# Kernel optimization log

Measured on AMD Instinct MI355X. Metric: run time of the kernel, lower is better.

## Reference

```python
import jax, jax.numpy as jnp
import numpy as np

N = 500_000      # total points
B = 64           # graphs in batch
D_IN = 64        # input feature dim (conv.in_tensor_reps.dim)
D_HID = 128      # EdgeConv MLP hidden
D_OUT = 128      # EdgeConv MLP out


def setup_inputs() -> dict:
    key = jax.random.key(0)
    k = jax.random.split(key, 8)
    x = jax.random.normal(k[0], (N, D_IN), jnp.float32)
    pos = jax.random.normal(k[1], (N, 3), jnp.float32)
    batch = jnp.sort(jax.random.randint(k[2], (N,), 0, B, dtype=jnp.int32))
    lframes = jax.random.normal(k[3], (N, 3, 3), jnp.float32)
    fan1 = 2 * D_IN + 3
    W1 = jax.random.normal(k[4], (fan1, D_HID), jnp.float32) / np.sqrt(fan1)
    b1 = jnp.zeros((D_HID,), jnp.float32)
    W2 = jax.random.normal(k[5], (D_HID, D_OUT), jnp.float32) / np.sqrt(D_HID)
    b2 = jnp.zeros((D_OUT,), jnp.float32)
    return {"x": x, "pos": pos, "batch": batch, "lframes": lframes,
            "W1": W1, "b1": b1, "W2": W2, "b2": b2}


def reference(x, pos, batch, lframes, W1, b1, W2, b2):
    n = pos.shape[0]
    # scatter-mean: center of mass per graph
    counts = jax.ops.segment_sum(jnp.ones((n,), pos.dtype), batch, num_segments=B)
    coms = jax.ops.segment_sum(pos, batch, num_segments=B) / jnp.maximum(counts, 1.0)[:, None]
    # distance of each point to its graph's COM
    dist = jnp.linalg.norm(pos - coms[batch], axis=-1)
    # scatter-min argmin per graph (first occurrence, like torch_scatter.scatter_min)
    min_d = jax.ops.segment_min(dist, batch, num_segments=B)
    node_ids = jnp.arange(n, dtype=jnp.int32)
    cand = jnp.where(dist <= min_d[batch], node_ids, n)
    idx = jnp.minimum(jax.ops.segment_min(cand, batch, num_segments=B), n - 1)  # [B]
    # gathers for the destination (center) nodes
    x_dst = x[idx]          # [B, D_IN]
    pos_dst = pos[idx]      # [B, 3]
    lframes_dst = lframes[idx]  # [B, 3, 3]
    # EdgeConv over edge_index = [arange(N) -> batch]:
    # message_e = MLP([x_dst_i, x_src_j - x_dst_i, pos_j - pos_i]), max-aggregated per graph
    xd = x_dst[batch]                      # [N, D_IN]
    feat = jnp.concatenate([xd, x - xd, pos - pos_dst[batch]], axis=-1)  # [N, 2*D_IN+3]
    h = jax.nn.relu(feat @ W1 + b1)        # [N, D_HID]
    msg = h @ W2 + b2                      # [N, D_OUT]
    out = jax.ops.segment_max(msg, batch, num_segments=B)  # [B, D_OUT]
    return out, pos_dst, batch[idx], lframes_dst
```

## Files before the change

kernel.cpp:

```cpp
#include <hip/hip_runtime.h>
#include <hip/hip_bf16.h>

#define NPTS 500000
#define NGR  64
#define TR   128
#define NT2  ((NPTS + TR - 1) / TR)
#define GRID2 1024

typedef __bf16 bf16x8 __attribute__((ext_vector_type(8)));
typedef float f32x4 __attribute__((ext_vector_type(4)));
typedef unsigned int u32x4 __attribute__((ext_vector_type(4)));

#define OFF_OUTACC 6144
#define OFF_CBIAS  38912
#define OFF_W1PT   71680
#define OFF_W1AT   73728
#define OFF_W2T    90112

__device__ __forceinline__ unsigned mapf(float f) {
    union { float f; unsigned u; } v; v.f = f;
    return ((int)v.u >= 0) ? (v.u | 0x80000000u) : ~v.u;
}

#define GLOAD_LDS16(g, l) __builtin_amdgcn_global_load_lds(                 \
    (__attribute__((address_space(1))) void*)(g),                           \
    (__attribute__((address_space(3))) void*)(l), 16, 0, 0)

__global__ __launch_bounds__(1024) void k_pre(
                      const float* __restrict__ pos,
                      const int* __restrict__ batch,
                      const float* __restrict__ x,
                      const float* __restrict__ W1,
                      const float* __restrict__ b1,
                      const float* __restrict__ W2,
                      const float* __restrict__ lfr,
                      unsigned short* __restrict__ W1aT,
                      unsigned short* __restrict__ W2T,
                      float* __restrict__ W1pT,
                      unsigned* __restrict__ outacc,
                      float* __restrict__ cbias,
                      float* __restrict__ outf) {
    __shared__ double sd[16][3];
    __shared__ unsigned long long sk[16];
    __shared__ double scom[3];
    __shared__ int sid;
    __shared__ float sposd[3];
    __shared__ float sp[4][128];
    __shared__ int sse[2];

    int g = blockIdx.x, t = threadIdx.x;
    int lane = t & 63, wv = t >> 6;

    {
        int i = g * 1024 + t;
        if (i < 8192) {
            outacc[i] = 0u;
            int n = i >> 6, k = i & 63;
            unsigned short v = (unsigned short)(__builtin_bit_cast(unsigned, (float)(__bf16)W1[(64 + k) * 128 + n]) >> 16);
            W1aT[i ^ ((n & 7) << 3)] = v;
        } else if (i < 8192 + 16384) {
            int j = i - 8192; int n = j >> 7, k = j & 127;
            unsigned short v = (unsigned short)(__builtin_bit_cast(unsigned, (float)(__bf16)W2[k * 128 + n]) >> 16);
            W2T[j ^ ((n & 7) << 3)] = v;
        } else if (i < 8192 + 16384 + 512) {
            int j = i - 24576; int n = j >> 2, q = j & 3;
            W1pT[j] = (q < 3) ? W1[(128 + q) * 128 + n] : 0.f;
        }
    }

    if (t < 2) {
        int target = g + t;
        int lo = 0, hi = NPTS;
        while (lo < hi) {
            int mid = (lo + hi) >> 1;
            if (batch[mid] < target) lo = mid + 1; else hi = mid;
        }
        sse[t] = lo;
    }
    __syncthreads();
    int s = sse[0], e = sse[1];

    double sx = 0.0, sy = 0.0, sz = 0.0;
    for (int i = s + t; i < e; i += 1024) {
        sx += (double)pos[i * 3 + 0];
        sy += (double)pos[i * 3 + 1];
        sz += (double)pos[i * 3 + 2];
    }
    #pragma unroll
    for (int m = 1; m < 64; m <<= 1) {
        sx += __shfl_xor(sx, m);
        sy += __shfl_xor(sy, m);
        sz += __shfl_xor(sz, m);
    }
    if (lane == 0) { sd[wv][0] = sx; sd[wv][1] = sy; sd[wv][2] = sz; }
    __syncthreads();
    if (t == 0) {
        double ax = 0.0, ay = 0.0, az = 0.0;
        for (int q = 0; q < 16; ++q) { ax += sd[q][0]; ay += sd[q][1]; az += sd[q][2]; }
        double cnt = (double)(e - s);
        double rc = 1.0 / (cnt > 1.0 ? cnt : 1.0);
        scom[0] = ax * rc; scom[1] = ay * rc; scom[2] = az * rc;
    }
    __syncthreads();
    double cx = scom[0], cy = scom[1], cz = scom[2];

    unsigned long long key = ~0ULL;
    for (int i = s + t; i < e; i += 1024) {
        double dx = (double)pos[i * 3 + 0] - cx;
        double dy = (double)pos[i * 3 + 1] - cy;
        double dz = (double)pos[i * 3 + 2] - cz;
        double d2 = __builtin_fma(dx, dx, __builtin_fma(dy, dy, dz * dz));
        unsigned long long b = __builtin_bit_cast(unsigned long long, d2);
        unsigned long long k2 = (b & ~0xFFFFFULL) | (unsigned long long)i;
        key = k2 < key ? k2 : key;
    }
    #pragma unroll
    for (int m = 1; m < 64; m <<= 1) {
        unsigned long long o = __shfl_xor(key, m);
        key = o < key ? o : key;
    }
    if (lane == 0) sk[wv] = key;
    __syncthreads();
    if (t == 0) {
        unsigned long long k = sk[0];
        for (int q = 1; q < 16; ++q) if (sk[q] < k) k = sk[q];
        int id = (int)(k & 0xFFFFFULL);
        if (id > NPTS - 1) id = NPTS - 1;
        sid = id;
    }
    __syncthreads();
    int id = sid;

    if (t < 3) {
        float p = pos[id * 3 + t];
        sposd[t] = p;
        outf[8192 + g * 3 + t] = p;
    }
    if (t == 4) outf[8192 + 192 + g] = (float)batch[id];
    if (t < 9) outf[8192 + 256 + g * 9 + t] = lfr[id * 9 + t];

    if (t < 512) {
        int c = t & 127, p = t >> 7;
        float part = 0.f;
        #pragma unroll
        for (int kq = 0; kq < 16; ++kq) {
            int k = p * 16 + kq;
            float xd = x[id * 64 + k];
            part += xd * (W1[k * 128 + c] - W1[(64 + k) * 128 + c]);
        }
        sp[p][c] = part;
    }
    __syncthreads();
    if (t < 128) {
        int c = t;
        float sv = b1[c] + sp[0][c] + sp[1][c] + sp[2][c] + sp[3][c];
        sv -= sposd[0] * W1[128 * 128 + c] + sposd[1] * W1[129 * 128 + c] + sposd[2] * W1[130 * 128 + c];
        cbias[g * 128 + c] = sv;
    }
}

__global__ __launch_bounds__(512, 2) void k_main(
    const float* __restrict__ x,
    const float* __restrict__ pos,
    const int* __restrict__ batch,
    const unsigned short* __restrict__ W1aT,
    const unsigned short* __restrict__ W2T,
    const float* __restrict__ W1pT,
    const float* __restrict__ cbias,
    unsigned* __restrict__ outacc)
{
    __shared__ alignas(16) unsigned char smem[81920];

    const int tid  = threadIdx.x;
    const int w    = tid >> 6;
    const int lane = tid & 63;
    const int quad = lane >> 4;
    const int mr   = lane & 15;

    #pragma unroll
    for (int i = 0; i < 6; ++i)
        GLOAD_LDS16((const char*)W1aT + (i * 512 + tid) * 16,
                    (char*)smem + (i * 512 + tid) * 16);

    bf16x8 bfrE[8];
    #pragma unroll
    for (int t8 = 0; t8 < 8; ++t8) {
        f32x4 wp = *(const f32x4*)(W1pT + (t8 * 16 + mr) * 4);
        bf16x8 e = (bf16x8){0, 0, 0, 0, 0, 0, 0, 0};
        if (quad == 0) { e[0] = (__bf16)wp[0]; e[1] = (__bf16)wp[1]; e[2] = (__bf16)wp[2]; }
        bfrE[t8] = e;
    }

    __syncthreads();

    const unsigned short* sW1 = (const unsigned short*)smem;
    const unsigned short* sW2 = (const unsigned short*)(smem + 16384);
    __bf16* hsb = (__bf16*)(smem + 49152) + w * 2048;
    const unsigned short* hss = (const unsigned short*)hsb;

    for (int t = blockIdx.x; t < NT2; t += GRID2) {
        const int row0 = t * TR + 16 * w;

        f32x4 av0, av1, av2, av3;
        {
            int gr2 = row0 + mr; if (gr2 > NPTS - 1) gr2 = NPTS - 1;
            const float* xp = x + (size_t)gr2 * 64 + quad * 8;
            av0 = *(const f32x4*)(xp);
            av1 = *(const f32x4*)(xp + 4);
            av2 = *(const f32x4*)(xp + 32);
            av3 = *(const f32x4*)(xp + 36);
        }

        int rowg[4]; bool rowv[4];
        #pragma unroll
        for (int r = 0; r < 4; ++r) {
            int gr = row0 + quad * 4 + r;
            rowv[r] = (gr < NPTS);
            rowg[r] = batch[gr < NPTS ? gr : NPTS - 1];
        }
        int gf = batch[row0 < NPTS ? row0 : NPTS - 1];
        int rl = row0 + 15; if (rl > NPTS - 1) rl = NPTS - 1;
        int gl = batch[rl];
        float cb0[8];
        #pragma unroll
        for (int t8 = 0; t8 < 8; ++t8) cb0[t8] = cbias[gf * 128 + t8 * 16 + mr];
        bf16x8 aE = (bf16x8){0, 0, 0, 0, 0, 0, 0, 0};
        {
            int gp = row0 + mr; if (gp > NPTS - 1) gp = NPTS - 1;
            if (quad == 0) {
                aE[0] = (__bf16)pos[gp * 3 + 0];
                aE[1] = (__bf16)pos[gp * 3 + 1];
                aE[2] = (__bf16)pos[gp * 3 + 2];
            }
        }

        bf16x8 afr0, afr1;
        afr0[0] = (__bf16)av0[0]; afr0[1] = (__bf16)av0[1]; afr0[2] = (__bf16)av0[2]; afr0[3] = (__bf16)av0[3];
        afr0[4] = (__bf16)av1[0]; afr0[5] = (__bf16)av1[1]; afr0[6] = (__bf16)av1[2]; afr0[7] = (__bf16)av1[3];
        afr1[0] = (__bf16)av2[0]; afr1[1] = (__bf16)av2[1]; afr1[2] = (__bf16)av2[2]; afr1[3] = (__bf16)av2[3];
        afr1[4] = (__bf16)av3[0]; afr1[5] = (__bf16)av3[1]; afr1[6] = (__bf16)av3[2]; afr1[7] = (__bf16)av3[3];

        f32x4 acc[8];
        #pragma unroll
        for (int t8 = 0; t8 < 8; ++t8) acc[t8] = (f32x4){0.f, 0.f, 0.f, 0.f};
        #pragma unroll
        for (int t8 = 0; t8 < 8; ++t8) {
            int n = t8 * 16 + mr;
            int sw = (n & 7) << 3;
            bf16x8 bv0 = __builtin_bit_cast(bf16x8, *(const u32x4*)(sW1 + ((n * 64 + quad * 8) ^ sw)));
            bf16x8 bv1 = __builtin_bit_cast(bf16x8, *(const u32x4*)(sW1 + ((n * 64 + 32 + quad * 8) ^ sw)));
            acc[t8] = __builtin_amdgcn_mfma_f32_16x16x32_bf16(afr0, bv0, acc[t8], 0, 0, 0);
            acc[t8] = __builtin_amdgcn_mfma_f32_16x16x32_bf16(afr1, bv1, acc[t8], 0, 0, 0);
            acc[t8] = __builtin_amdgcn_mfma_f32_16x16x32_bf16(aE, bfrE[t8], acc[t8], 0, 0, 0);
        }

        #pragma unroll
        for (int r = 0; r < 4; ++r) {
            int lrow = quad * 4 + r;
            int g = rowg[r];
            bool odd = (g != gf);
            int sw = (lrow & 7) << 3;
            #pragma unroll
            for (int t8 = 0; t8 < 8; ++t8) {
                float cbv = cb0[t8];
                if (odd) cbv = cbias[g * 128 + t8 * 16 + mr];
                float v = fmaxf(acc[t8][r] + cbv, 0.f);
                hsb[lrow * 128 + ((t8 * 16 + mr) ^ sw)] = (__bf16)v;
            }
        }

        f32x4 acc2[8];
        #pragma unroll
        for (int t8 = 0; t8 < 8; ++t8) acc2[t8] = (f32x4){0.f, 0.f, 0.f, 0.f};
        int swr = (mr & 7) << 3;
        #pragma unroll
        for (int kk = 0; kk < 4; ++kk) {
            bf16x8 a2 = __builtin_bit_cast(bf16x8,
                *(const u32x4*)(hss + mr * 128 + ((kk * 32 + quad * 8) ^ swr)));
            #pragma unroll
            for (int t8 = 0; t8 < 8; ++t8) {
                int n = t8 * 16 + mr;
                bf16x8 bv = __builtin_bit_cast(bf16x8,
                    *(const u32x4*)(sW2 + ((n * 128 + kk * 32 + quad * 8) ^ ((n & 7) << 3))));
                acc2[t8] = __builtin_amdgcn_mfma_f32_16x16x32_bf16(a2, bv, acc2[t8], 0, 0, 0);
            }
        }

        for (int g = gf; g <= gl; ++g) {
            #pragma unroll
            for (int t8 = 0; t8 < 8; ++t8) {
                float m = -INFINITY;
                #pragma unroll
                for (int r = 0; r < 4; ++r)
                    if (rowv[r] && rowg[r] == g) m = fmaxf(m, acc2[t8][r]);
                m = fmaxf(m, __shfl_xor(m, 16));
                m = fmaxf(m, __shfl_xor(m, 32));
                unsigned mb = __builtin_bit_cast(unsigned, m);
                if (quad == 0 && mb != 0xFF800000u)
                    atomicMax(&outacc[g * 128 + t8 * 16 + mr], mapf(m));
            }
        }
    }
}

__global__ void k_out(const unsigned* __restrict__ outacc,
                      const float* __restrict__ b2v,
                      float* __restrict__ outf) {
    int i = blockIdx.x * 256 + threadIdx.x;
    unsigned key = outacc[i];
    float v;
    if (key == 0u) {
        v = -300.f;
    } else {
        unsigned bits = (key & 0x80000000u) ? (key & 0x7FFFFFFFu) : ~key;
        union { unsigned u; float f; } c; c.u = bits; v = c.f;
    }
    outf[i] = v + b2v[i & 127];
}

extern "C" void kernel_launch(void* const* d_in, const int* in_sizes, int n_in,
                              void* d_out, int out_size, void* d_ws, size_t ws_size,
                              hipStream_t stream) {
    const float* x   = (const float*)d_in[0];
    const float* pos = (const float*)d_in[1];
    const int*   bat = (const int*)d_in[2];
    const float* lfr = (const float*)d_in[3];
    const float* W1  = (const float*)d_in[4];
    const float* b1  = (const float*)d_in[5];
    const float* W2  = (const float*)d_in[6];
    const float* b2v = (const float*)d_in[7];
    float* outf = (float*)d_out;

    char* ws = (char*)d_ws;
    unsigned*       outacc = (unsigned*)(ws + OFF_OUTACC);
    float*          cbias  = (float*)(ws + OFF_CBIAS);
    float*          W1pT   = (float*)(ws + OFF_W1PT);
    unsigned short* W1aT   = (unsigned short*)(ws + OFF_W1AT);
    unsigned short* W2T    = (unsigned short*)(ws + OFF_W2T);

    k_pre<<<64, 1024, 0, stream>>>(pos, bat, x, W1, b1, W2, lfr,
                                   W1aT, W2T, W1pT, outacc, cbias, outf);
    k_main<<<GRID2, 512, 0, stream>>>(x, pos, bat, W1aT, W2T, W1pT, cbias, outacc);
    k_out<<<32, 256, 0, stream>>>(outacc, b2v, outf);
}
```

Before: 300.8 us.

## Prefetch next tile's x and pos in registers with contiguous chunked tiles

The persistent grid-stride loop over tiles becomes contiguous chunks of four tiles per block, launching about 977 blocks instead of 1024. Inside each chunk the x and pos loads for the next tile are issued before the current tile's MFMA work, software-pipelining the global loads against compute. The cost is extra live registers, which may reduce occupancy, plus a per-block prologue setup that is now amortised over only four tiles.

Result: faster. 275.6 us (-8.4%).

```diff
diff --git a/kernel.cpp b/kernel.cpp
--- a/kernel.cpp
+++ b/kernel.cpp
@@ -5,7 +5,8 @@
 #define NGR  64
 #define TR   128
 #define NT2  ((NPTS + TR - 1) / TR)
-#define GRID2 1024
+#define CHUNK 4
+#define NBLK ((NT2 + CHUNK - 1) / CHUNK)
 
 typedef __bf16 bf16x8 __attribute__((ext_vector_type(8)));
 typedef float f32x4 __attribute__((ext_vector_type(4)));
@@ -198,47 +199,61 @@
     __bf16* hsb = (__bf16*)(smem + 49152) + w * 2048;
     const unsigned short* hss = (const unsigned short*)hsb;
 
-    for (int t = blockIdx.x; t < NT2; t += GRID2) {
+    const int tb = blockIdx.x * CHUNK;
+    int te = tb + CHUNK; if (te > NT2) te = NT2;
+
+    f32x4 av0, av1, av2, av3;
+    float pv0, pv1, pv2;
+    {
+        int gr = tb * TR + 16 * w + mr; if (gr > NPTS - 1) gr = NPTS - 1;
+        const float* xp = x + (size_t)gr * 64 + quad * 8;
+        av0 = *(const f32x4*)(xp);
+        av1 = *(const f32x4*)(xp + 4);
+        av2 = *(const f32x4*)(xp + 32);
+        av3 = *(const f32x4*)(xp + 36);
+        pv0 = pos[gr * 3 + 0];
+        pv1 = pos[gr * 3 + 1];
+        pv2 = pos[gr * 3 + 2];
+    }
+
+    for (int t = tb; t < te; ++t) {
         const int row0 = t * TR + 16 * w;
-
-        f32x4 av0, av1, av2, av3;
-        {
-            int gr2 = row0 + mr; if (gr2 > NPTS - 1) gr2 = NPTS - 1;
-            const float* xp = x + (size_t)gr2 * 64 + quad * 8;
-            av0 = *(const f32x4*)(xp);
-            av1 = *(const f32x4*)(xp + 4);
-            av2 = *(const f32x4*)(xp + 32);
-            av3 = *(const f32x4*)(xp + 36);
-        }
-
-        int rowg[4]; bool rowv[4];
-        #pragma unroll
-        for (int r = 0; r < 4; ++r) {
-            int gr = row0 + quad * 4 + r;
-            rowv[r] = (gr < NPTS);
-            rowg[r] = batch[gr < NPTS ? gr : NPTS - 1];
-        }
-        int gf = batch[row0 < NPTS ? row0 : NPTS - 1];
-        int rl = row0 + 15; if (rl > NPTS - 1) rl = NPTS - 1;
-        int gl = batch[rl];
-        float cb0[8];
-        #pragma unroll
-        for (int t8 = 0; t8 < 8; ++t8) cb0[t8] = cbias[gf * 128 + t8 * 16 + mr];
-        bf16x8 aE = (bf16x8){0, 0, 0, 0, 0, 0, 0, 0};
-        {
-            int gp = row0 + mr; if (gp > NPTS - 1) gp = NPTS - 1;
-            if (quad == 0) {
-                aE[0] = (__bf16)pos[gp * 3 + 0];
-                aE[1] = (__bf16)pos[gp * 3 + 1];
-                aE[2] = (__bf16)pos[gp * 3 + 2];
-            }
-        }
 
         bf16x8 afr0, afr1;
         afr0[0] = (__bf16)av0[0]; afr0[1] = (__bf16)av0[1]; afr0[2] = (__bf16)av0[2]; afr0[3] = (__bf16)av0[3];
         afr0[4] = (__bf16)av1[0]; afr0[5] = (__bf16)av1[1]; afr0[6] = (__bf16)av1[2]; afr0[7] = (__bf16)av1[3];
         afr1[0] = (__bf16)av2[0]; afr1[1] = (__bf16)av2[1]; afr1[2] = (__bf16)av2[2]; afr1[3] = (__bf16)av2[3];
         afr1[4] = (__bf16)av3[0]; afr1[5] = (__bf16)av3[1]; afr1[6] = (__bf16)av3[2]; afr1[7] = (__bf16)av3[3];
+        bf16x8 aE = (bf16x8){0, 0, 0, 0, 0, 0, 0, 0};
+        if (quad == 0) {
+            aE[0] = (__bf16)pv0; aE[1] = (__bf16)pv1; aE[2] = (__bf16)pv2;
+        }
+
+        if (t + 1 < te) {
+            int gr = (t + 1) * TR + 16 * w + mr; if (gr > NPTS - 1) gr = NPTS - 1;
+            const float* xp = x + (size_t)gr * 64 + quad * 8;
+            av0 = *(const f32x4*)(xp);
+            av1 = *(const f32x4*)(xp + 4);
+            av2 = *(const f32x4*)(xp + 32);
+            av3 = *(const f32x4*)(xp + 36);
+            pv0 = pos[gr * 3 + 0];
+            pv1 = pos[gr * 3 + 1];
+            pv2 = pos[gr * 3 + 2];
+        }
+
+        int rowg[4]; bool rowv[4];
+        #pragma unroll
+        for (int r = 0; r < 4; ++r) {
+            int gr = row0 + quad * 4 + r;
+            rowv[r] = (gr < NPTS);
+            rowg[r] = batch[gr < NPTS ? gr : NPTS - 1];
+        }
+        int gf = batch[row0 < NPTS ? row0 : NPTS - 1];
+        int rl = row0 + 15; if (rl > NPTS - 1) rl = NPTS - 1;
+        int gl = batch[rl];
+        float cb0[8];
+        #pragma unroll
+        for (int t8 = 0; t8 < 8; ++t8) cb0[t8] = cbias[gf * 128 + t8 * 16 + mr];
 
         f32x4 acc[8];
         #pragma unroll
@@ -340,6 +355,6 @@
 
     k_pre<<<64, 1024, 0, stream>>>(pos, bat, x, W1, b1, W2, lfr,
                                    W1aT, W2T, W1pT, outacc, cbias, outf);
-    k_main<<<GRID2, 512, 0, stream>>>(x, pos, bat, W1aT, W2T, W1pT, cbias, outacc);
+    k_main<<<NBLK, 512, 0, stream>>>(x, pos, bat, W1aT, W2T, W1pT, cbias, outacc);
     k_out<<<32, 256, 0, stream>>>(outacc, b2v, outf);
 }
```
